# Kernel optimization log

Hardware: AMD Instinct MI355X
Metric: run time of the kernel (lower is better)

The kernel has to match this reference:

```python
import jax, jax.numpy as jnp
import numpy as np

T = 15          # fixed window length from docstring
CENTER = 7      # center_idx
MAXL = 8        # max_len_f = max_len_b = 8
B, D, H = 8192, 512, 512


def _gru_final(x, lengths, Wih, Whh, bih, bhh):
    """Run a GRU over x (B, L, D) and return the hidden state after each
    sample's own `lengths` steps (packed-sequence final-hidden semantics)."""
    Bn, L, _ = x.shape
    Hn = Whh.shape[1]
    # Precompute input projections for all timesteps: (B, L, 3H)
    xp = jnp.einsum('bld,gd->blg', x, Wih) + bih
    mask = jnp.arange(L)[None, :] < lengths[:, None]  # (B, L) valid steps

    def step(h, inp):
        xp_t, m_t = inp                      # (B,3H), (B,)
        gh = h @ Whh.T + bhh                 # (B,3H)
        xr, xz, xn = jnp.split(xp_t, 3, axis=-1)
        hr, hz, hn = jnp.split(gh, 3, axis=-1)
        r = jax.nn.sigmoid(xr + hr)
        z = jax.nn.sigmoid(xz + hz)
        n = jnp.tanh(xn + r * hn)
        h_new = (1.0 - z) * n + z * h
        h = jnp.where(m_t[:, None], h_new, h)  # freeze h past sequence end
        return h, None

    h0 = jnp.zeros((Bn, Hn), x.dtype)
    hT, _ = jax.lax.scan(step, h0, (jnp.moveaxis(xp, 0, 1)[:L], mask.T))
    return hT


def setup_inputs() -> dict:
    key = jax.random.key(0)
    ks = jax.random.split(key, 16)
    s_ih = 1.0 / np.sqrt(H)
    u = lambda k, shape: jax.random.uniform(k, shape, jnp.float32, -s_ih, s_ih)
    inp = {
        'padded_window': jax.random.normal(ks[0], (B, T, D), jnp.float32),
        'window_len': jax.random.randint(ks[1], (B,), 1, T + 1, jnp.int32),
        # forward GRU params (PyTorch layout: gates ordered r,z,n)
        'Wih_f': u(ks[2], (3 * H, D)), 'Whh_f': u(ks[3], (3 * H, H)),
        'bih_f': u(ks[4], (3 * H,)),   'bhh_f': u(ks[5], (3 * H,)),
        # backward GRU params
        'Wih_b': u(ks[6], (3 * H, D)), 'Whh_b': u(ks[7], (3 * H, H)),
        'bih_b': u(ks[8], (3 * H,)),   'bhh_b': u(ks[9], (3 * H,)),
        # MLP: Linear(2H,H) -> ReLU -> Linear(H,H)
        'W1': u(ks[10], (H, 2 * H)), 'b1': u(ks[11], (H,)),
        'W2': u(ks[12], (H, H)),     'b2': u(ks[13], (H,)),
    }
    return inp


def reference(padded_window, window_len, Wih_f, Whh_f, bih_f, bhh_f,
              Wih_b, Whh_b, bih_b, bhh_b, W1, b1, W2, b2):
    len_f = (window_len - 1) // 2 + 1   # (B,)
    len_b = window_len // 2 + 1         # (B,)
    j = jnp.arange(MAXL)
    # forward sub-sequence: window[center-l_f+1 : center+1]
    idx_f = jnp.clip(CENTER - len_f[:, None] + 1 + j[None, :], 0, T - 1)
    # backward sub-sequence: flip(window[center : center+l_b]) -> descending idx
    idx_b = jnp.clip(CENTER + len_b[:, None] - 1 - j[None, :], 0, T - 1)
    xf = jnp.take_along_axis(padded_window, idx_f[:, :, None], axis=1)  # (B,8,D)
    xb = jnp.take_along_axis(padded_window, idx_b[:, :, None], axis=1)  # (B,8,D)
    h_f = _gru_final(xf, len_f, Wih_f, Whh_f, bih_f, bhh_f)
    h_b = _gru_final(xb, len_b, Wih_b, Whh_b, bih_b, bhh_b)
    combined = jnp.concatenate([h_f, h_b], axis=1)  # (B, 2H)
    hidden = jax.nn.relu(combined @ W1.T + b1)
    return hidden @ W2.T + b2
```

## Files before the change

### kernel.cpp

```cpp
#include <hip/hip_runtime.h>

typedef unsigned short u16;
typedef __attribute__((ext_vector_type(4))) float f32x4;
typedef __attribute__((ext_vector_type(8))) __bf16 bf16x8;
typedef __attribute__((ext_vector_type(8))) u16 u16x8;
typedef __attribute__((ext_vector_type(4))) u16 u16x4;
typedef __attribute__((ext_vector_type(4))) int i32x4;

#define MFMA(a, b, c) __builtin_amdgcn_mfma_f32_16x16x32_bf16(a, b, c, 0, 0, 0)

__device__ __forceinline__ u16 f2bf(float f) {
  union { float f; unsigned u; } v; v.f = f;
  unsigned r = v.u + 0x7FFFu + ((v.u >> 16) & 1u);
  return (u16)(r >> 16);
}
__device__ __forceinline__ float bf2f(u16 b) {
  union { unsigned u; float f; } v; v.u = ((unsigned)b) << 16; return v.f;
}
__device__ __forceinline__ float sigm(float x) { return 1.f / (1.f + __expf(-x)); }
__device__ __forceinline__ float tanh_(float x) {
  float e = __expf(-2.f * fabsf(x));
  float r = (1.f - e) / (1.f + e);
  return x < 0.f ? -r : r;
}

#define GSTRIDE 131072

__global__ __launch_bounds__(256) void cvt_bf16(const float* __restrict__ src,
                                                u16* __restrict__ dst, int n8) {
  int i = blockIdx.x * 256 + threadIdx.x;
  if (i >= n8) return;
  int e = i * 8;
  u16x8 o;
#pragma unroll
  for (int j = 0; j < 8; ++j) o[j] = f2bf(src[e + j]);
  *(u16x8*)(dst + e) = o;
}

__global__ __launch_bounds__(256) void wrepack(const float* __restrict__ Whh,
                                               u16* __restrict__ Wp) {
  int i = blockIdx.x * 256 + threadIdx.x;
  if (i >= 98304) return;
  int q = i / 3072;
  int r1 = i % 3072;
  int kk = r1 / 192;
  int r2 = r1 % 192;
  int g = r2 / 64;
  int r3 = r2 % 64;
  int ks = r3 >> 4, ln = r3 & 15;
  const float* src =
      Whh + (size_t)(g * 512 + q * 16 + ln) * 512 + kk * 32 + ks * 8;
  u16x8 o;
#pragma unroll
  for (int j = 0; j < 8; ++j) o[j] = f2bf(src[j]);
  *(u16x8*)(Wp + (size_t)i * 8) = o;
}

__global__ __launch_bounds__(1024) void sort_len(const int* __restrict__ wlen,
                                                 int* __restrict__ order) {
  __shared__ int cnt[16];
  __shared__ int off[16];
  const int tid = threadIdx.x;
  if (tid < 16) cnt[tid] = 0;
  __syncthreads();
  for (int i = tid; i < 8192; i += 1024) atomicAdd(&cnt[wlen[i] - 1], 1);
  __syncthreads();
  if (tid == 0) {
    int run = 0;
#pragma unroll
    for (int b = 0; b < 15; ++b) { off[b] = run; run += cnt[b]; }
  }
  __syncthreads();
  for (int i = tid; i < 8192; i += 1024) {
    int pos = atomicAdd(&off[wlen[i] - 1], 1);
    order[pos] = i;
  }
}

#define LROWA 520

__global__ __launch_bounds__(256)
__attribute__((amdgpu_waves_per_eu(1, 1))) void xp_gemm(
    const float* __restrict__ win, const int* __restrict__ wlen,
    const int* __restrict__ order, const u16* __restrict__ Wihb_f,
    const u16* __restrict__ Wihb_b, const float* __restrict__ bih_f,
    const float* __restrict__ bih_b, const float* __restrict__ bhh_f,
    const float* __restrict__ bhh_b, u16* __restrict__ xp) {
  extern __shared__ char smem[];
  u16* As = (u16*)smem;

  const int dir = blockIdx.z;
  const int t = blockIdx.y;
  const int sbase = blockIdx.x * 128;

  {
    int wl_last = wlen[order[sbase + 127]];
    int len_last = dir ? (wl_last / 2 + 1) : ((wl_last - 1) / 2 + 1);
    if (len_last <= t) return;
  }

  const u16* Wb = dir ? Wihb_b : Wihb_f;
  const float* bih = dir ? bih_b : bih_f;
  const float* bhh = dir ? bhh_b : bhh_f;

  const int tid = threadIdx.x;

  {
    const int r = tid >> 1, hh = tid & 1;
    const int sample = order[sbase + r];
    const int wl = wlen[sample];
    const int len = dir ? (wl / 2 + 1) : ((wl - 1) / 2 + 1);
    const int widx = dir ? (6 + len - t) : (8 - len + t);
    const float* src = win + ((size_t)sample * 15 + widx) * 512 + hh * 256;
    u16* dst = As + r * LROWA + hh * 256;
#pragma unroll
    for (int i = 0; i < 32; ++i) {
      f32x4 v0 = *(const f32x4*)(src + i * 8);
      f32x4 v1 = *(const f32x4*)(src + i * 8 + 4);
      u16x8 o;
      o[0] = f2bf(v0[0]); o[1] = f2bf(v0[1]); o[2] = f2bf(v0[2]); o[3] = f2bf(v0[3]);
      o[4] = f2bf(v1[0]); o[5] = f2bf(v1[1]); o[6] = f2bf(v1[2]); o[7] = f2bf(v1[3]);
      *(u16x8*)(dst + i * 8) = o;
    }
  }
  __syncthreads();

  const int wave = tid >> 6;
  const int lane = tid & 63;
  const int ln = lane & 15;
  const int ks = lane >> 4;

#pragma unroll 1
  for (int g = 0; g < 6; ++g) {
    const int c0 = wave * 24 + g * 4;

    f32x4 acc[8][4];
#pragma unroll
    for (int mt = 0; mt < 8; ++mt)
#pragma unroll
      for (int u = 0; u < 4; ++u)
#pragma unroll
        for (int j = 0; j < 4; ++j) acc[mt][u][j] = 0.f;

#pragma unroll
    for (int kk = 0; kk < 16; ++kk) {
      const int krel = kk * 32 + ks * 8;
      bf16x8 a[8];
#pragma unroll
      for (int mt = 0; mt < 8; ++mt)
        a[mt] = *(const bf16x8*)(As + (mt * 16 + ln) * LROWA + krel);
      bf16x8 b[4];
#pragma unroll
      for (int u = 0; u < 4; ++u)
        b[u] = *(const bf16x8*)(Wb + (size_t)((c0 + u) * 16 + ln) * 512 + krel);
#pragma unroll
      for (int mt = 0; mt < 8; ++mt)
#pragma unroll
        for (int u = 0; u < 4; ++u) acc[mt][u] = MFMA(a[mt], b[u], acc[mt][u]);
    }

#pragma unroll
    for (int u = 0; u < 4; ++u) {
      const int col = (c0 + u) * 16 + ln;
      const float bv = bih[col] + (col < 1024 ? bhh[col] : 0.f);
#pragma unroll
      for (int mt = 0; mt < 8; ++mt)
#pragma unroll
        for (int j = 0; j < 4; ++j) {
          const int slot = sbase + mt * 16 + ks * 4 + j;
          const size_t idx = ((size_t)(dir * 8 + t) * 96 + (c0 + u)) * GSTRIDE +
                             (size_t)(slot >> 2) * 64 + ln * 4 + (slot & 3);
          xp[idx] = f2bf(acc[mt][u][j] + bv);
        }
    }
  }
}

#define LROW 520

__global__ __launch_bounds__(1024)
__attribute__((amdgpu_waves_per_eu(4, 4))) void gru_rec(
    const int* __restrict__ wlen, const int* __restrict__ order,
    const u16* __restrict__ Wp_f, const u16* __restrict__ Wp_b,
    const float* __restrict__ bhh_f, const float* __restrict__ bhh_b,
    const u16* __restrict__ xp, u16* __restrict__ hcat) {
  extern __shared__ char smem[];
  u16* hb0 = (u16*)smem;
  u16* hb1 = hb0 + 64 * LROW;
  int* len_s = (int*)(hb1 + 64 * LROW);
  int* bmax_s = len_s + 64;

  const int dir = blockIdx.x & 1;
  const int grp = blockIdx.x >> 1;
  const int s0 = grp * 64;
  const u16* W = dir ? Wp_b : Wp_f;
  const float* bhh = dir ? bhh_b : bhh_f;

  const int tid = threadIdx.x;
  const int wave = tid >> 6;
  const int lane = tid & 63;
  const int ln = lane & 15;
  const int ks = lane >> 4;

  if (tid == 0) *bmax_s = 0;
  for (int i = tid; i < 64 * LROW / 8; i += 1024) ((u16x8*)hb0)[i] = (u16x8)0;
  __syncthreads();
  if (tid < 64) {
    int wl = wlen[order[s0 + tid]];
    int len = dir ? (wl / 2 + 1) : ((wl - 1) / 2 + 1);
    len_s[tid] = len;
    atomicMax(bmax_s, len);
  }
  __syncthreads();
  const int bmax = *bmax_s;

  float b_hn[2];
#pragma unroll
  for (int p = 0; p < 2; ++p) b_hn[p] = bhh[1024 + (p * 16 + wave) * 16 + ln];

  for (int t = 0; t < bmax; ++t) {
    u16* h_cur = (t & 1) ? hb1 : hb0;
    u16* h_nxt = (t & 1) ? hb0 : hb1;
    const u16* xpt = xp + (size_t)(dir * 8 + t) * 96 * GSTRIDE;

#pragma unroll
    for (int p = 0; p < 2; ++p) {
      const int q = p * 16 + wave;
      const int dcol = q * 16 + ln;
      const u16* wq = W + (size_t)q * 24576 + lane * 8;

      u16x4 xr4[4], xz4[4], xn4[4];
#pragma unroll
      for (int mt = 0; mt < 4; ++mt) {
        const size_t off = (size_t)((s0 >> 2) + mt * 4 + ks) * 64 + ln * 4;
        xr4[mt] = *(const u16x4*)(xpt + (size_t)q * GSTRIDE + off);
        xz4[mt] = *(const u16x4*)(xpt + (size_t)(32 + q) * GSTRIDE + off);
        xn4[mt] = *(const u16x4*)(xpt + (size_t)(64 + q) * GSTRIDE + off);
      }

      f32x4 accr[4], accz[4], acchn[4];
#pragma unroll
      for (int mt = 0; mt < 4; ++mt)
#pragma unroll
        for (int j = 0; j < 4; ++j) {
          accr[mt][j] = 0.f; accz[mt][j] = 0.f; acchn[mt][j] = 0.f;
        }

#pragma unroll
      for (int kk = 0; kk < 16; ++kk) {
        const int krel = kk * 32 + ks * 8;
        bf16x8 a[4];
#pragma unroll
        for (int mt = 0; mt < 4; ++mt)
          a[mt] = *(const bf16x8*)(h_cur + (mt * 16 + ln) * LROW + krel);
        const u16* wk = wq + kk * 1536;
        bf16x8 br = *(const bf16x8*)(wk);
        bf16x8 bz = *(const bf16x8*)(wk + 512);
        bf16x8 bn = *(const bf16x8*)(wk + 1024);
#pragma unroll
        for (int mt = 0; mt < 4; ++mt) {
          accr[mt] = MFMA(a[mt], br, accr[mt]);
          accz[mt] = MFMA(a[mt], bz, accz[mt]);
          acchn[mt] = MFMA(a[mt], bn, acchn[mt]);
        }
      }

#pragma unroll
      for (int mt = 0; mt < 4; ++mt)
#pragma unroll
        for (int j = 0; j < 4; ++j) {
          const int row = mt * 16 + ks * 4 + j;
          float xr = bf2f(xr4[mt][j]);
          float xz = bf2f(xz4[mt][j]);
          float xn = bf2f(xn4[mt][j]);
          float rr = sigm(accr[mt][j] + xr);
          float zz = sigm(accz[mt][j] + xz);
          float nn = tanh_(xn + rr * (acchn[mt][j] + b_hn[p]));
          float hold = bf2f(h_cur[row * LROW + dcol]);
          float hnew = (t < len_s[row]) ? ((1.f - zz) * nn + zz * hold) : hold;
          h_nxt[row * LROW + dcol] = f2bf(hnew);
        }
    }
    __syncthreads();
  }

  const u16* hf = (bmax & 1) ? hb1 : hb0;
  const int xrow = tid >> 4;
  const int xcol = tid & 15;
#pragma unroll
  for (int i = 0; i < 4; ++i) {
    int off = (i * 16 + xcol) * 8;
    u16x8 v = *(const u16x8*)(hf + xrow * LROW + off);
    __builtin_nontemporal_store(
        v, (u16x8*)(hcat + (size_t)(s0 + xrow) * 1024 + dir * 512 + off));
  }
}

__global__ __launch_bounds__(256) void build_wcat(const float* __restrict__ Whh,
                                                  const float* __restrict__ Wih,
                                                  u16* __restrict__ Wcat) {
  int i = blockIdx.x * 256 + threadIdx.x;
  if (i >= 1536 * 1024 / 8) return;
  int e = i * 8;
  int g = e >> 10, k = e & 1023;
  const float* src = (k < 512) ? (Whh + g * 512 + k) : (Wih + g * 512 + (k - 512));
  u16x8 o;
#pragma unroll
  for (int j = 0; j < 8; ++j) o[j] = f2bf(src[j]);
  *(u16x8*)(Wcat + e) = o;
}

__global__ __launch_bounds__(512)
__attribute__((amdgpu_waves_per_eu(2, 2))) void gru_persistent(
    const float* __restrict__ win, const int* __restrict__ wlen,
    const u16* __restrict__ Wcat_f, const u16* __restrict__ Wcat_b,
    const float* __restrict__ bih_f, const float* __restrict__ bhh_f,
    const float* __restrict__ bih_b, const float* __restrict__ bhh_b,
    u16* __restrict__ hcat) {
  extern __shared__ char smem[];
  u16* h_s = (u16*)smem;
  u16* x_s = (u16*)(smem + 64 * LROW * 2);
  int* len_s = (int*)(smem + 2 * 64 * LROW * 2);
  int* bmax_s = len_s + 64;

  const int dir = blockIdx.x & 1;
  const int grp = blockIdx.x >> 1;
  const int s0 = grp * 64;
  const u16* W = dir ? Wcat_b : Wcat_f;
  const float* bih = dir ? bih_b : bih_f;
  const float* bhh = dir ? bhh_b : bhh_f;

  const int tid = threadIdx.x;
  const int wave = tid >> 6;
  const int lane = tid & 63;
  const int ln = lane & 15;
  const int ks = lane >> 4;

  if (tid == 0) *bmax_s = 0;
  for (int i = tid; i < 64 * LROW / 8; i += 512) ((u16x8*)h_s)[i] = (u16x8)0;
  __syncthreads();
  if (tid < 64) {
    int wl = wlen[s0 + tid];
    int len = dir ? (wl / 2 + 1) : ((wl - 1) / 2 + 1);
    len_s[tid] = len;
    atomicMax(bmax_s, len);
  }
  __syncthreads();
  const int bmax = *bmax_s;

  float b_r[4], b_z[4], b_xn[4], b_hn[4];
#pragma unroll
  for (int p = 0; p < 4; ++p) {
    int d = (p * 8 + wave) * 16 + ln;
    b_r[p] = bih[d] + bhh[d];
    b_z[p] = bih[512 + d] + bhh[512 + d];
    b_xn[p] = bih[1024 + d];
    b_hn[p] = bhh[1024 + d];
  }

  const int xrow = tid >> 3;
  const int xcol = tid & 7;
  const int mylen = len_s[xrow];
  const long xbase = (long)(s0 + xrow) * 15 + (dir ? (6 + mylen) : (8 - mylen));

  for (int t = 0; t < bmax; ++t) {
    {
      long rowidx = dir ? (xbase - t) : (xbase + t);
      const float* src = win + rowidx * 512;
      u16* dst = x_s + xrow * LROW;
#pragma unroll
      for (int i = 0; i < 8; ++i) {
        int off = xcol * 8 + i * 64;
        f32x4 v0 = *(const f32x4*)(src + off);
        f32x4 v1 = *(const f32x4*)(src + off + 4);
        u16x8 o;
        o[0] = f2bf(v0[0]); o[1] = f2bf(v0[1]); o[2] = f2bf(v0[2]); o[3] = f2bf(v0[3]);
        o[4] = f2bf(v1[0]); o[5] = f2bf(v1[1]); o[6] = f2bf(v1[2]); o[7] = f2bf(v1[3]);
        *(u16x8*)(dst + off) = o;
      }
    }
    __syncthreads();

    unsigned holdp[3][4][2];

#pragma unroll
    for (int p = 0; p < 4; ++p) {
      const int dcol = (p * 8 + wave) * 16 + ln;
      const u16* wrow = W + (size_t)dcol * 1024;

      f32x4 accr[4], accz[4], acchn[4], accxn[4];
#pragma unroll
      for (int mt = 0; mt < 4; ++mt)
#pragma unroll
        for (int j = 0; j < 4; ++j) {
          accr[mt][j] = 0.f; accz[mt][j] = 0.f;
          acchn[mt][j] = 0.f; accxn[mt][j] = 0.f;
        }

#pragma unroll
      for (int kk = 0; kk < 16; ++kk) {
        const int krel = kk * 32 + ks * 8;
        bf16x8 a[4];
#pragma unroll
        for (int mt = 0; mt < 4; ++mt)
          a[mt] = *(const bf16x8*)(h_s + (mt * 16 + ln) * LROW + krel);
        bf16x8 br = *(const bf16x8*)(wrow + krel);
        bf16x8 bz = *(const bf16x8*)(wrow + 512 * 1024 + krel);
        bf16x8 bn = *(const bf16x8*)(wrow + 1024 * 1024 + krel);
#pragma unroll
        for (int mt = 0; mt < 4; ++mt) {
          accr[mt] = MFMA(a[mt], br, accr[mt]);
          accz[mt] = MFMA(a[mt], bz, accz[mt]);
          acchn[mt] = MFMA(a[mt], bn, acchn[mt]);
        }
      }
#pragma unroll
      for (int kk = 0; kk < 16; ++kk) {
        const int krel = kk * 32 + ks * 8;
        bf16x8 a[4];
#pragma unroll
        for (int mt = 0; mt < 4; ++mt)
          a[mt] = *(const bf16x8*)(x_s + (mt * 16 + ln) * LROW + krel);
        bf16x8 br = *(const bf16x8*)(wrow + 512 + krel);
        bf16x8 bz = *(const bf16x8*)(wrow + 512 * 1024 + 512 + krel);
        bf16x8 bn = *(const bf16x8*)(wrow + 1024 * 1024 + 512 + krel);
#pragma unroll
        for (int mt = 0; mt < 4; ++mt) {
          accr[mt] = MFMA(a[mt], br, accr[mt]);
          accz[mt] = MFMA(a[mt], bz, accz[mt]);
          accxn[mt] = MFMA(a[mt], bn, accxn[mt]);
        }
      }

      if (p < 3) {
#pragma unroll
        for (int mt = 0; mt < 4; ++mt)
#pragma unroll
          for (int jp = 0; jp < 2; ++jp) {
            unsigned pk = 0;
#pragma unroll
            for (int jh = 0; jh < 2; ++jh) {
              const int j = jp * 2 + jh;
              const int row = mt * 16 + ks * 4 + j;
              float rr = sigm(accr[mt][j] + b_r[p]);
              float zz = sigm(accz[mt][j] + b_z[p]);
              float nn = tanh_(accxn[mt][j] + b_xn[p] +
                               rr * (acchn[mt][j] + b_hn[p]));
              float hold = bf2f(h_s[row * LROW + dcol]);
              float hnew = (t < len_s[row]) ? ((1.f - zz) * nn + zz * hold) : hold;
              pk |= ((unsigned)f2bf(hnew)) << (16 * jh);
            }
            holdp[p][mt][jp] = pk;
          }
      } else {
        __syncthreads();
#pragma unroll
        for (int pp = 0; pp < 3; ++pp) {
          const int dd = (pp * 8 + wave) * 16 + ln;
#pragma unroll
          for (int mt = 0; mt < 4; ++mt)
#pragma unroll
            for (int jp = 0; jp < 2; ++jp) {
              unsigned pk = holdp[pp][mt][jp];
              const int row = mt * 16 + ks * 4 + jp * 2;
              h_s[row * LROW + dd] = (u16)pk;
              h_s[(row + 1) * LROW + dd] = (u16)(pk >> 16);
            }
        }
#pragma unroll
        for (int mt = 0; mt < 4; ++mt)
#pragma unroll
          for (int j = 0; j < 4; ++j) {
            const int row = mt * 16 + ks * 4 + j;
            float rr = sigm(accr[mt][j] + b_r[3]);
            float zz = sigm(accz[mt][j] + b_z[3]);
            float nn = tanh_(accxn[mt][j] + b_xn[3] +
                             rr * (acchn[mt][j] + b_hn[3]));
            float hold = bf2f(h_s[row * LROW + dcol]);
            float hnew = (t < len_s[row]) ? ((1.f - zz) * nn + zz * hold) : hold;
            h_s[row * LROW + dcol] = f2bf(hnew);
          }
      }
    }
  }

  __syncthreads();
#pragma unroll
  for (int i = 0; i < 8; ++i) {
    int off = xcol * 8 + i * 64;
    u16x8 v = *(const u16x8*)(h_s + xrow * LROW + off);
    __builtin_nontemporal_store(
        v, (u16x8*)(hcat + (size_t)(s0 + xrow) * 1024 + dir * 512 + off));
  }
}

__global__ __launch_bounds__(256) void mlp_gemm(const u16* __restrict__ A,
                                                const u16* __restrict__ Bw,
                                                const float* __restrict__ bias,
                                                const int* __restrict__ perm,
                                                void* __restrict__ out, int M,
                                                int N, int K, int mode) {
  __shared__ u16 As[128 * 64], Bs[128 * 64];
  const int tid = threadIdx.x;
  const int wave = tid >> 6, lane = tid & 63;
  const int ln = lane & 15, ks = lane >> 4;
  const int wm = wave & 1, wn = wave >> 1;
  const int m0 = blockIdx.x * 128, n0 = blockIdx.y * 128;
  f32x4 acc[4][4];
#pragma unroll
  for (int mt = 0; mt < 4; ++mt)
#pragma unroll
    for (int nt = 0; nt < 4; ++nt)
#pragma unroll
      for (int j = 0; j < 4; ++j) acc[mt][nt][j] = 0.f;

  const int r = tid >> 1, hh = tid & 1;
  for (int k0 = 0; k0 < K; k0 += 64) {
    const i32x4* sa = (const i32x4*)(A + (size_t)(m0 + r) * K + k0 + hh * 32);
    const i32x4* sb = (const i32x4*)(Bw + (size_t)(n0 + r) * K + k0 + hh * 32);
    i32x4* da = (i32x4*)(As + r * 64 + hh * 32);
    i32x4* db = (i32x4*)(Bs + r * 64 + hh * 32);
#pragma unroll
    for (int i = 0; i < 4; ++i) da[i] = sa[i];
#pragma unroll
    for (int i = 0; i < 4; ++i) db[i] = sb[i];
    __syncthreads();
#pragma unroll
    for (int kk = 0; kk < 2; ++kk) {
      bf16x8 af[4], bfm[4];
#pragma unroll
      for (int mt = 0; mt < 4; ++mt)
        af[mt] = *(const bf16x8*)(As + (wm * 64 + mt * 16 + ln) * 64 + kk * 32 + ks * 8);
#pragma unroll
      for (int nt = 0; nt < 4; ++nt)
        bfm[nt] = *(const bf16x8*)(Bs + (wn * 64 + nt * 16 + ln) * 64 + kk * 32 + ks * 8);
#pragma unroll
      for (int mt = 0; mt < 4; ++mt)
#pragma unroll
        for (int nt = 0; nt < 4; ++nt) acc[mt][nt] = MFMA(af[mt], bfm[nt], acc[mt][nt]);
    }
    __syncthreads();
  }

#pragma unroll
  for (int nt = 0; nt < 4; ++nt) {
    int col = n0 + wn * 64 + nt * 16 + ln;
    float bv = bias[col];
#pragma unroll
    for (int mt = 0; mt < 4; ++mt)
#pragma unroll
      for (int j = 0; j < 4; ++j) {
        int row = m0 + wm * 64 + mt * 16 + ks * 4 + j;
        float v = acc[mt][nt][j] + bv;
        int orow = perm ? perm[row] : row;
        if (mode) {
          v = fmaxf(v, 0.f);
          ((u16*)out)[(size_t)orow * N + col] = f2bf(v);
        } else {
          ((float*)out)[(size_t)orow * N + col] = v;
        }
      }
  }
}

extern "C" void kernel_launch(void* const* d_in, const int* in_sizes, int n_in,
                              void* d_out, int out_size, void* d_ws, size_t ws_size,
                              hipStream_t stream) {
  (void)in_sizes; (void)n_in; (void)out_size;
  const float* win = (const float*)d_in[0];
  const int* wlen = (const int*)d_in[1];
  const float* Wih_f = (const float*)d_in[2];
  const float* Whh_f = (const float*)d_in[3];
  const float* bih_f = (const float*)d_in[4];
  const float* bhh_f = (const float*)d_in[5];
  const float* Wih_b = (const float*)d_in[6];
  const float* Whh_b = (const float*)d_in[7];
  const float* bih_b = (const float*)d_in[8];
  const float* bhh_b = (const float*)d_in[9];
  const float* W1 = (const float*)d_in[10];
  const float* b1 = (const float*)d_in[11];
  const float* W2 = (const float*)d_in[12];
  const float* b2 = (const float*)d_in[13];

  const size_t NEED = 4ull * 1572864 + 1048576 + 524288 + 16777216 + 8388608 +
                      402653184ull + 32768;

  if (ws_size >= NEED) {
    char* ws = (char*)d_ws;
    u16* Wp_f = (u16*)ws;   ws += 1572864;
    u16* Wp_b = (u16*)ws;   ws += 1572864;
    u16* Wihb_f = (u16*)ws; ws += 1572864;
    u16* Wihb_b = (u16*)ws; ws += 1572864;
    u16* W1b = (u16*)ws;    ws += 1048576;
    u16* W2b = (u16*)ws;    ws += 524288;
    u16* hcat = (u16*)ws;   ws += 16777216;
    u16* hidden = (u16*)ws; ws += 8388608;
    int* order = (int*)ws;  ws += 32768;
    u16* xp = (u16*)ws;     ws += 402653184;

    sort_len<<<1, 1024, 0, stream>>>(wlen, order);
    wrepack<<<384, 256, 0, stream>>>(Whh_f, Wp_f);
    wrepack<<<384, 256, 0, stream>>>(Whh_b, Wp_b);
    cvt_bf16<<<384, 256, 0, stream>>>(Wih_f, Wihb_f, 98304);
    cvt_bf16<<<384, 256, 0, stream>>>(Wih_b, Wihb_b, 98304);
    cvt_bf16<<<256, 256, 0, stream>>>(W1, W1b, 65536);
    cvt_bf16<<<128, 256, 0, stream>>>(W2, W2b, 32768);

    const int SMEM_XP = 128 * LROWA * 2;
    (void)hipFuncSetAttribute((const void*)xp_gemm,
                              hipFuncAttributeMaxDynamicSharedMemorySize, SMEM_XP);
    xp_gemm<<<dim3(64, 8, 2), 256, SMEM_XP, stream>>>(
        win, wlen, order, Wihb_f, Wihb_b, bih_f, bih_b, bhh_f, bhh_b, xp);

    const int SMEM = 2 * 64 * LROW * 2 + 64 * 4 + 16;
    (void)hipFuncSetAttribute((const void*)gru_rec,
                              hipFuncAttributeMaxDynamicSharedMemorySize, SMEM);
    gru_rec<<<256, 1024, SMEM, stream>>>(wlen, order, Wp_f, Wp_b, bhh_f, bhh_b,
                                         xp, hcat);

    mlp_gemm<<<dim3(64, 4), 256, 0, stream>>>(hcat, W1b, b1, nullptr, hidden,
                                              8192, 512, 1024, 1);
    mlp_gemm<<<dim3(64, 4), 256, 0, stream>>>(hidden, W2b, b2, order, d_out,
                                              8192, 512, 512, 0);
  } else {
    char* ws = (char*)d_ws;
    u16* Wcat_f = (u16*)ws;  ws += 3145728;
    u16* Wcat_b = (u16*)ws;  ws += 3145728;
    u16* W1b = (u16*)ws;     ws += 1048576;
    u16* W2b = (u16*)ws;     ws += 524288;
    u16* hcat = (u16*)ws;    ws += 16777216;
    u16* hidden = (u16*)ws;  ws += 8388608;

    build_wcat<<<768, 256, 0, stream>>>(Whh_f, Wih_f, Wcat_f);
    build_wcat<<<768, 256, 0, stream>>>(Whh_b, Wih_b, Wcat_b);
    cvt_bf16<<<256, 256, 0, stream>>>(W1, W1b, 65536);
    cvt_bf16<<<128, 256, 0, stream>>>(W2, W2b, 32768);

    const int SMEM = 2 * 64 * LROW * 2 + 64 * 4 + 16;
    (void)hipFuncSetAttribute((const void*)gru_persistent,
                              hipFuncAttributeMaxDynamicSharedMemorySize, SMEM);
    gru_persistent<<<256, 512, SMEM, stream>>>(win, wlen, Wcat_f, Wcat_b, bih_f,
                                               bhh_f, bih_b, bhh_b, hcat);

    mlp_gemm<<<dim3(64, 4), 256, 0, stream>>>(hcat, W1b, b1, nullptr, hidden,
                                              8192, 512, 1024, 1);
    mlp_gemm<<<dim3(64, 4), 256, 0, stream>>>(hidden, W2b, b2, nullptr, d_out,
                                              8192, 512, 512, 0);
  }
}
```

Baseline: 1.947 ms.

## Tile xp GEMM over unsorted sample-timestep rows with rank-based scatter

Reorganises the input-projection GEMM so each block takes 64 consecutive (sample, timestep) rows in original sample order, instead of 128 sorted samples at one fixed timestep. The output is scattered to its sorted slot through a new rank array that sort_len now writes. Blocks are smaller and twice as many can fit per EU, which improves occupancy and makes input reads contiguous. The cost is dropping the early exit for blocks past the sequence length, so padded timesteps are now always computed, and the output stores become more scattered.

```diff
diff --git a/kernel.cpp b/kernel.cpp
--- a/kernel.cpp
+++ b/kernel.cpp
@@ -57,7 +57,8 @@
 }
 
 __global__ __launch_bounds__(1024) void sort_len(const int* __restrict__ wlen,
-                                                 int* __restrict__ order) {
+                                                 int* __restrict__ order,
+                                                 int* __restrict__ rank) {
   __shared__ int cnt[16];
   __shared__ int off[16];
   const int tid = threadIdx.x;
@@ -74,47 +75,41 @@
   for (int i = tid; i < 8192; i += 1024) {
     int pos = atomicAdd(&off[wlen[i] - 1], 1);
     order[pos] = i;
+    rank[i] = pos;
   }
 }
 
 #define LROWA 520
 
 __global__ __launch_bounds__(256)
-__attribute__((amdgpu_waves_per_eu(1, 1))) void xp_gemm(
+__attribute__((amdgpu_waves_per_eu(2, 2))) void xp_gemm(
     const float* __restrict__ win, const int* __restrict__ wlen,
-    const int* __restrict__ order, const u16* __restrict__ Wihb_f,
+    const int* __restrict__ rank, const u16* __restrict__ Wihb_f,
     const u16* __restrict__ Wihb_b, const float* __restrict__ bih_f,
     const float* __restrict__ bih_b, const float* __restrict__ bhh_f,
     const float* __restrict__ bhh_b, u16* __restrict__ xp) {
   extern __shared__ char smem[];
   u16* As = (u16*)smem;
 
-  const int dir = blockIdx.z;
-  const int t = blockIdx.y;
-  const int sbase = blockIdx.x * 128;
-
-  {
-    int wl_last = wlen[order[sbase + 127]];
-    int len_last = dir ? (wl_last / 2 + 1) : ((wl_last - 1) / 2 + 1);
-    if (len_last <= t) return;
-  }
-
+  const int dir = blockIdx.y;
   const u16* Wb = dir ? Wihb_b : Wihb_f;
   const float* bih = dir ? bih_b : bih_f;
   const float* bhh = dir ? bhh_b : bhh_f;
 
   const int tid = threadIdx.x;
+  const int bx = blockIdx.x;
 
   {
-    const int r = tid >> 1, hh = tid & 1;
-    const int sample = order[sbase + r];
-    const int wl = wlen[sample];
+    const int r = tid >> 2, qq = tid & 3;
+    const int m = bx * 64 + r;
+    const int s = m >> 3, tt = m & 7;
+    const int wl = wlen[s];
     const int len = dir ? (wl / 2 + 1) : ((wl - 1) / 2 + 1);
-    const int widx = dir ? (6 + len - t) : (8 - len + t);
-    const float* src = win + ((size_t)sample * 15 + widx) * 512 + hh * 256;
-    u16* dst = As + r * LROWA + hh * 256;
-#pragma unroll
-    for (int i = 0; i < 32; ++i) {
+    const int widx = dir ? (6 + len - tt) : (8 - len + tt);
+    const float* src = win + ((size_t)s * 15 + widx) * 512 + qq * 128;
+    u16* dst = As + r * LROWA + qq * 128;
+#pragma unroll
+    for (int i = 0; i < 16; ++i) {
       f32x4 v0 = *(const f32x4*)(src + i * 8);
       f32x4 v1 = *(const f32x4*)(src + i * 8 + 4);
       u16x8 o;
@@ -134,9 +129,9 @@
   for (int g = 0; g < 6; ++g) {
     const int c0 = wave * 24 + g * 4;
 
-    f32x4 acc[8][4];
-#pragma unroll
-    for (int mt = 0; mt < 8; ++mt)
+    f32x4 acc[4][4];
+#pragma unroll
+    for (int mt = 0; mt < 4; ++mt)
 #pragma unroll
       for (int u = 0; u < 4; ++u)
 #pragma unroll
@@ -145,16 +140,16 @@
 #pragma unroll
     for (int kk = 0; kk < 16; ++kk) {
       const int krel = kk * 32 + ks * 8;
-      bf16x8 a[8];
-#pragma unroll
-      for (int mt = 0; mt < 8; ++mt)
+      bf16x8 a[4];
+#pragma unroll
+      for (int mt = 0; mt < 4; ++mt)
         a[mt] = *(const bf16x8*)(As + (mt * 16 + ln) * LROWA + krel);
       bf16x8 b[4];
 #pragma unroll
       for (int u = 0; u < 4; ++u)
         b[u] = *(const bf16x8*)(Wb + (size_t)((c0 + u) * 16 + ln) * 512 + krel);
 #pragma unroll
-      for (int mt = 0; mt < 8; ++mt)
+      for (int mt = 0; mt < 4; ++mt)
 #pragma unroll
         for (int u = 0; u < 4; ++u) acc[mt][u] = MFMA(a[mt], b[u], acc[mt][u]);
     }
@@ -164,10 +159,12 @@
       const int col = (c0 + u) * 16 + ln;
       const float bv = bih[col] + (col < 1024 ? bhh[col] : 0.f);
 #pragma unroll
-      for (int mt = 0; mt < 8; ++mt)
+      for (int mt = 0; mt < 4; ++mt)
 #pragma unroll
         for (int j = 0; j < 4; ++j) {
-          const int slot = sbase + mt * 16 + ks * 4 + j;
+          const int m2 = bx * 64 + mt * 16 + ks * 4 + j;
+          const int s = m2 >> 3, t = m2 & 7;
+          const int slot = rank[s];
           const size_t idx = ((size_t)(dir * 8 + t) * 96 + (c0 + u)) * GSTRIDE +
                              (size_t)(slot >> 2) * 64 + ln * 4 + (slot & 3);
           xp[idx] = f2bf(acc[mt][u][j] + bv);
@@ -583,7 +580,7 @@
   const float* b2 = (const float*)d_in[13];
 
   const size_t NEED = 4ull * 1572864 + 1048576 + 524288 + 16777216 + 8388608 +
-                      402653184ull + 32768;
+                      402653184ull + 65536;
 
   if (ws_size >= NEED) {
     char* ws = (char*)d_ws;
@@ -596,9 +593,10 @@
     u16* hcat = (u16*)ws;   ws += 16777216;
     u16* hidden = (u16*)ws; ws += 8388608;
     int* order = (int*)ws;  ws += 32768;
+    int* rank = (int*)ws;   ws += 32768;
     u16* xp = (u16*)ws;     ws += 402653184;
 
-    sort_len<<<1, 1024, 0, stream>>>(wlen, order);
+    sort_len<<<1, 1024, 0, stream>>>(wlen, order, rank);
     wrepack<<<384, 256, 0, stream>>>(Whh_f, Wp_f);
     wrepack<<<384, 256, 0, stream>>>(Whh_b, Wp_b);
     cvt_bf16<<<384, 256, 0, stream>>>(Wih_f, Wihb_f, 98304);
@@ -606,11 +604,11 @@
     cvt_bf16<<<256, 256, 0, stream>>>(W1, W1b, 65536);
     cvt_bf16<<<128, 256, 0, stream>>>(W2, W2b, 32768);
 
-    const int SMEM_XP = 128 * LROWA * 2;
+    const int SMEM_XP = 64 * LROWA * 2;
     (void)hipFuncSetAttribute((const void*)xp_gemm,
                               hipFuncAttributeMaxDynamicSharedMemorySize, SMEM_XP);
-    xp_gemm<<<dim3(64, 8, 2), 256, SMEM_XP, stream>>>(
-        win, wlen, order, Wihb_f, Wihb_b, bih_f, bih_b, bhh_f, bhh_b, xp);
+    xp_gemm<<<dim3(1024, 2), 256, SMEM_XP, stream>>>(
+        win, wlen, rank, Wihb_f, Wihb_b, bih_f, bih_b, bhh_f, bhh_b, xp);
 
     const int SMEM = 2 * 64 * LROW * 2 + 64 * 4 + 16;
     (void)hipFuncSetAttribute((const void*)gru_rec,
```

Measured after the change: 2.226 ms. 14.3% more time.
